# Kernel tuning notes

Hardware: AMD Instinct MI355X
Metric: run time of the kernel (lower is better)

## Reference

```python
import jax, jax.numpy as jnp
import numpy as np

B, T, U, D, V = 8, 200, 100, 512, 1024


def setup_inputs() -> dict:
    key = jax.random.key(0)
    k1, k2, k3, k4 = jax.random.split(key, 4)
    enc_out = jax.random.normal(k1, (B, T, D), dtype=jnp.float32)
    prefix = jax.random.randint(k2, (B, U), 0, V, dtype=jnp.int64)
    embedding = jax.random.normal(k3, (V, D), dtype=jnp.float32)
    joiner_w = jax.random.normal(k4, (V, D), dtype=jnp.float32) * (1.0 / np.sqrt(D))
    joiner_b = jnp.zeros((V,), dtype=jnp.float32)
    return {"enc_out": enc_out, "prefix": prefix, "embedding": embedding,
            "joiner_w": joiner_w, "joiner_b": joiner_b}


def reference(enc_out, prefix, embedding, joiner_w, joiner_b):
    # pred_emb: (B, U, D) via embedding lookup
    pred_emb = embedding[prefix]
    # broadcast add -> (B, T, U, D), then tanh
    joint = jnp.tanh(enc_out[:, :, None, :] + pred_emb[:, None, :, :])
    # linear projection to vocab: (B, T, U, V)
    logits = jnp.einsum('btud,vd->btuv', joint, joiner_w) + joiner_b
    return logits
```

## Files before the change

kernel.cpp:

```cpp
#include <hip/hip_runtime.h>

#define T_DIM 200
#define U_DIM 100
#define D_DIM 512
#define V_DIM 1024
#define TU_DIM (T_DIM * U_DIM)
#define M_TOTAL (8 * TU_DIM)
#define M_TILE 64

typedef __attribute__((ext_vector_type(8))) short bf16x8;
typedef __attribute__((ext_vector_type(4))) float f32x4;

__device__ __forceinline__ unsigned short f2bf(float f) {
    unsigned int u = __float_as_uint(f);
    u += 0x7FFFu + ((u >> 16) & 1u);
    return (unsigned short)(u >> 16);
}

__device__ __forceinline__ float fast_tanh(float x) {
    float e = __expf(2.0f * x);
    return 1.0f - 2.0f / (e + 1.0f);
}

__device__ __forceinline__ void row_ptrs(int g, const float* enc, const int* prefix,
                                         const float* emb, const float** encp, const float** embp) {
    const int b = g / TU_DIM;
    const int m = g - b * TU_DIM;
    const int t = m / U_DIM;
    const int u = m - t * U_DIM;
    *encp = enc + (size_t)(b * T_DIM + t) * D_DIM;
    *embp = emb + (size_t)prefix[b * U_DIM + u] * D_DIM;
}

__global__ void conv_w_kernel(const float* __restrict__ w, ushort4* __restrict__ wbf) {
    int i = blockIdx.x * blockDim.x + threadIdx.x;
    float4 v = reinterpret_cast<const float4*>(w)[i];
    ushort4 o;
    o.x = f2bf(v.x); o.y = f2bf(v.y); o.z = f2bf(v.z); o.w = f2bf(v.w);
    wbf[i] = o;
}

__global__ __launch_bounds__(512)
void mat_a_kernel(const float* __restrict__ enc, const int* __restrict__ prefix,
                  const float* __restrict__ emb, unsigned short* __restrict__ Abf) {
    const int tid = threadIdx.x;
    const int r = tid >> 3;
    const int q = tid & 7;
    const int rl = blockIdx.x * 64 + r;
    const float *encp, *embp;
    row_ptrs(rl, enc, prefix, emb, &encp, &embp);
    unsigned short* ap = Abf + (size_t)rl * D_DIM;
#pragma unroll
    for (int jj = 0; jj < 8; ++jj) {
        const int d = q * 8 + jj * 64;
        float4 e0 = *reinterpret_cast<const float4*>(encp + d);
        float4 e1 = *reinterpret_cast<const float4*>(encp + d + 4);
        float4 p0 = *reinterpret_cast<const float4*>(embp + d);
        float4 p1 = *reinterpret_cast<const float4*>(embp + d + 4);
        bf16x8 pk;
        pk[0] = (short)f2bf(fast_tanh(e0.x + p0.x));
        pk[1] = (short)f2bf(fast_tanh(e0.y + p0.y));
        pk[2] = (short)f2bf(fast_tanh(e0.z + p0.z));
        pk[3] = (short)f2bf(fast_tanh(e0.w + p0.w));
        pk[4] = (short)f2bf(fast_tanh(e1.x + p1.x));
        pk[5] = (short)f2bf(fast_tanh(e1.y + p1.y));
        pk[6] = (short)f2bf(fast_tanh(e1.z + p1.z));
        pk[7] = (short)f2bf(fast_tanh(e1.w + p1.w));
        *reinterpret_cast<bf16x8*>(&ap[d]) = pk;
    }
}

#define GLOAD_LDS16(gp, lp) \
    __builtin_amdgcn_global_load_lds( \
        (const __attribute__((address_space(1))) unsigned int*)(gp), \
        (__attribute__((address_space(3))) unsigned int*)(lp), 16, 0, 0)

__global__ __launch_bounds__(512, 2)
void gemm8_kernel(const unsigned short* __restrict__ Abf, const unsigned short* __restrict__ wbf,
                  const float* __restrict__ bias, float* __restrict__ out) {
    __shared__ unsigned short ldsA[2][256 * 64];
    __shared__ unsigned short ldsB[2][256 * 64];

    const int tid  = threadIdx.x;
    const int lane = tid & 63;
    const int wid  = tid >> 6;
    const int wm   = wid >> 2;
    const int wn   = wid & 3;
    const int lr   = lane & 15;
    const int lg   = lane >> 4;

    const int orig = blockIdx.x;
    const int xcd = orig & 7;
    const int wgid = (xcd < 4 ? xcd * 313 : 4 * 313 + (xcd - 4) * 312) + (orig >> 3);
    const int mt = wgid >> 2, nt = wgid & 3;
    const int row0 = mt * 256, col0 = nt * 256;

    const int rsub = tid >> 3;
    const int csw  = ((tid & 7) ^ (rsub & 7)) * 8;

    const unsigned short* aSt = Abf + (size_t)(row0 + rsub) * D_DIM + csw;
    const unsigned short* wSt = wbf + (size_t)(col0 + rsub) * D_DIM + csw;

    const unsigned short* ldsA0 = &ldsA[0][(wm * 128 + lr) * 64 + ((lg ^ (lr & 7)) * 8)];
    const unsigned short* ldsB0 = &ldsB[0][(wn * 64 + lr) * 64 + ((lg ^ (lr & 7)) * 8)];
    const int kk1off = ((((4 | lg) ^ (lr & 7)) - (lg ^ (lr & 7))) * 8);

    f32x4 acc[8][4];
#pragma unroll
    for (int mi = 0; mi < 8; ++mi)
#pragma unroll
        for (int ni = 0; ni < 4; ++ni)
            acc[mi][ni] = (f32x4){0.f, 0.f, 0.f, 0.f};

    auto stage = [&](int buf) {
#pragma unroll
        for (int j = 0; j < 4; ++j)
            GLOAD_LDS16(aSt + (size_t)j * (64 * D_DIM), &ldsA[buf][(j * 64 + wid * 8) * 64]);
#pragma unroll
        for (int j = 0; j < 4; ++j)
            GLOAD_LDS16(wSt + (size_t)j * (64 * D_DIM), &ldsB[buf][(j * 64 + wid * 8) * 64]);
        aSt += 64;
        wSt += 64;
    };

    auto compute = [&](int buf) {
        const unsigned short* pA = ldsA0 + buf * (256 * 64);
        const unsigned short* pB = ldsB0 + buf * (256 * 64);
#pragma unroll
        for (int kk = 0; kk < 2; ++kk) {
            const int ko = kk ? kk1off : 0;
            bf16x8 bfr[4];
#pragma unroll
            for (int ni = 0; ni < 4; ++ni)
                bfr[ni] = *reinterpret_cast<const bf16x8*>(pB + ni * (16 * 64) + ko);
            __builtin_amdgcn_s_setprio(1);
#pragma unroll
            for (int mi = 0; mi < 8; ++mi) {
                bf16x8 af = *reinterpret_cast<const bf16x8*>(pA + mi * (16 * 64) + ko);
#pragma unroll
                for (int ni = 0; ni < 4; ++ni)
                    acc[mi][ni] = __builtin_amdgcn_mfma_f32_16x16x32_bf16(af, bfr[ni], acc[mi][ni], 0, 0, 0);
            }
            __builtin_amdgcn_s_setprio(0);
        }
    };

    stage(0);
    stage(1);

#pragma unroll 1
    for (int it = 0; it < 4; ++it) {
        asm volatile("s_waitcnt vmcnt(8)" ::: "memory");
        __builtin_amdgcn_s_barrier();
        compute(0);
        asm volatile("s_waitcnt lgkmcnt(0)" ::: "memory");
        __builtin_amdgcn_s_barrier();
        if (it < 3) stage(0);
        if (it < 3) asm volatile("s_waitcnt vmcnt(8)" ::: "memory");
        else        asm volatile("s_waitcnt vmcnt(0)" ::: "memory");
        __builtin_amdgcn_s_barrier();
        compute(1);
        if (it < 3) {
            asm volatile("s_waitcnt lgkmcnt(0)" ::: "memory");
            __builtin_amdgcn_s_barrier();
            stage(1);
        }
    }

    float bv[4];
#pragma unroll
    for (int ni = 0; ni < 4; ++ni)
        bv[ni] = bias[col0 + wn * 64 + ni * 16 + lr];
#pragma unroll
    for (int mi = 0; mi < 8; ++mi) {
#pragma unroll
        for (int j = 0; j < 4; ++j) {
            const long long row = (long long)row0 + wm * 128 + mi * 16 + lg * 4 + j;
            float* op = out + row * V_DIM + col0 + wn * 64;
#pragma unroll
            for (int ni = 0; ni < 4; ++ni)
                __builtin_nontemporal_store(acc[mi][ni][j] + bv[ni], &op[ni * 16 + lr]);
        }
    }
}

__global__ __launch_bounds__(512, 2)
void joiner_kernel(const float* __restrict__ enc, const int* __restrict__ prefix,
                   const float* __restrict__ emb, const unsigned short* __restrict__ wbf,
                   const float* __restrict__ bias, float* __restrict__ out) {
    __shared__ unsigned short A_s[M_TILE * 512];
    const int tid = threadIdx.x;
    const long long g0 = (long long)blockIdx.x * M_TILE;
    {
        const int r = tid >> 3, q = tid & 7;
        const float *encp, *embp;
        row_ptrs((int)g0 + r, enc, prefix, emb, &encp, &embp);
        const int r7 = r & 7;
#pragma unroll
        for (int jj = 0; jj < 8; ++jj) {
            const int d = q * 8 + jj * 64;
            float4 e0 = *reinterpret_cast<const float4*>(encp + d);
            float4 e1 = *reinterpret_cast<const float4*>(encp + d + 4);
            float4 p0 = *reinterpret_cast<const float4*>(embp + d);
            float4 p1 = *reinterpret_cast<const float4*>(embp + d + 4);
            bf16x8 pk;
            pk[0] = (short)f2bf(fast_tanh(e0.x + p0.x));
            pk[1] = (short)f2bf(fast_tanh(e0.y + p0.y));
            pk[2] = (short)f2bf(fast_tanh(e0.z + p0.z));
            pk[3] = (short)f2bf(fast_tanh(e0.w + p0.w));
            pk[4] = (short)f2bf(fast_tanh(e1.x + p1.x));
            pk[5] = (short)f2bf(fast_tanh(e1.y + p1.y));
            pk[6] = (short)f2bf(fast_tanh(e1.z + p1.z));
            pk[7] = (short)f2bf(fast_tanh(e1.w + p1.w));
            const int chunk = (q + 8 * jj) ^ r7;
            *reinterpret_cast<bf16x8*>(&A_s[r * 512 + chunk * 8]) = pk;
        }
    }
    __syncthreads();
    const int lane = tid & 63, wid = tid >> 6;
    const int wn = wid * 128, lr = lane & 15, lg = lane >> 4;
    const unsigned short* wb = wbf + (size_t)(wn + lr) * D_DIM + lg * 8;
    f32x4 acc[4][8];
#pragma unroll
    for (int mi = 0; mi < 4; ++mi)
#pragma unroll
        for (int ni = 0; ni < 8; ++ni) acc[mi][ni] = (f32x4){0.f, 0.f, 0.f, 0.f};
    bf16x8 bb[2][8];
#pragma unroll
    for (int ni = 0; ni < 8; ++ni)
        bb[0][ni] = *reinterpret_cast<const bf16x8*>(wb + ni * 16 * D_DIM);
#pragma unroll
    for (int s = 0; s < 16; ++s) {
        const int cur = s & 1, nxt = cur ^ 1;
        if (s < 15) {
#pragma unroll
            for (int ni = 0; ni < 8; ++ni)
                bb[nxt][ni] = *reinterpret_cast<const bf16x8*>(wb + ni * 16 * D_DIM + (s + 1) * 32);
        }
        bf16x8 af[4];
#pragma unroll
        for (int mi = 0; mi < 4; ++mi) {
            const int row = mi * 16 + lr;
            const int chunk = (s * 4 + lg) ^ (row & 7);
            af[mi] = *reinterpret_cast<const bf16x8*>(&A_s[row * 512 + chunk * 8]);
        }
#pragma unroll
        for (int mi = 0; mi < 4; ++mi)
#pragma unroll
            for (int ni = 0; ni < 8; ++ni)
                acc[mi][ni] = __builtin_amdgcn_mfma_f32_16x16x32_bf16(af[mi], bb[cur][ni], acc[mi][ni], 0, 0, 0);
    }
    float bv[8];
#pragma unroll
    for (int ni = 0; ni < 8; ++ni) bv[ni] = bias[wn + ni * 16 + lr];
#pragma unroll
    for (int mi = 0; mi < 4; ++mi) {
#pragma unroll
        for (int j = 0; j < 4; ++j) {
            const long long row = g0 + mi * 16 + lg * 4 + j;
            float* op = out + row * V_DIM + wn;
#pragma unroll
            for (int ni = 0; ni < 8; ++ni)
                op[ni * 16 + lr] = acc[mi][ni][j] + bv[ni];
        }
    }
}

extern "C" void kernel_launch(void* const* d_in, const int* in_sizes, int n_in,
                              void* d_out, int out_size, void* d_ws, size_t ws_size,
                              hipStream_t stream) {
    const float* enc    = (const float*)d_in[0];
    const int*   prefix = (const int*)d_in[1];
    const float* emb    = (const float*)d_in[2];
    const float* jw     = (const float*)d_in[3];
    const float* jb     = (const float*)d_in[4];
    float* out = (float*)d_out;

    unsigned short* wbf = (unsigned short*)d_ws;
    const size_t WB = (size_t)V_DIM * D_DIM * sizeof(unsigned short);
    const size_t AB = (size_t)M_TOTAL * D_DIM * sizeof(unsigned short);

    conv_w_kernel<<<512, 256, 0, stream>>>(jw, (ushort4*)wbf);

    if (ws_size >= WB + AB) {
        unsigned short* Abf = wbf + (size_t)V_DIM * D_DIM;
        mat_a_kernel<<<M_TOTAL / 64, 512, 0, stream>>>(enc, prefix, emb, Abf);
        gemm8_kernel<<<2500, 512, 0, stream>>>(Abf, wbf, jb, out);
    } else {
        joiner_kernel<<<M_TOTAL / M_TILE, 512, 0, stream>>>(enc, prefix, emb, wbf, jb, out);
    }
}
```

Before: 284.0 us.

## Shrink GEMM tile to 128x128 with four waves and more workgroups

Replaces the 256x256-tile, 8-wave GEMM with a 128x128-tile, 4-wave kernel launched over 10000 workgroups, with a simpler XCD-aware remapping of block ids to tiles. Smaller tiles use less LDS and fewer registers per block. That should allow more resident blocks and better load balance across CUs, and shrink the tail of the grid. In exchange, arithmetic intensity per tile drops, so A and W are re-read from L2 more often.

```diff
diff --git a/kernel.cpp b/kernel.cpp
--- a/kernel.cpp
+++ b/kernel.cpp
@@ -75,57 +75,56 @@
         (const __attribute__((address_space(1))) unsigned int*)(gp), \
         (__attribute__((address_space(3))) unsigned int*)(lp), 16, 0, 0)
 
-__global__ __launch_bounds__(512, 2)
-void gemm8_kernel(const unsigned short* __restrict__ Abf, const unsigned short* __restrict__ wbf,
-                  const float* __restrict__ bias, float* __restrict__ out) {
-    __shared__ unsigned short ldsA[2][256 * 64];
-    __shared__ unsigned short ldsB[2][256 * 64];
+__global__ __launch_bounds__(256, 2)
+void gemm128_kernel(const unsigned short* __restrict__ Abf, const unsigned short* __restrict__ wbf,
+                    const float* __restrict__ bias, float* __restrict__ out) {
+    __shared__ unsigned short ldsA[2][128 * 64];
+    __shared__ unsigned short ldsB[2][128 * 64];
 
     const int tid  = threadIdx.x;
     const int lane = tid & 63;
     const int wid  = tid >> 6;
-    const int wm   = wid >> 2;
-    const int wn   = wid & 3;
+    const int wm   = (wid >> 1) * 64;
+    const int wn   = (wid & 1) * 64;
     const int lr   = lane & 15;
     const int lg   = lane >> 4;
 
     const int orig = blockIdx.x;
-    const int xcd = orig & 7;
-    const int wgid = (xcd < 4 ? xcd * 313 : 4 * 313 + (xcd - 4) * 312) + (orig >> 3);
-    const int mt = wgid >> 2, nt = wgid & 3;
-    const int row0 = mt * 256, col0 = nt * 256;
+    const int wgid = (orig & 7) * 1250 + (orig >> 3);
+    const int mt = wgid >> 3, nt = wgid & 7;
+    const int row0 = mt * 128, col0 = nt * 128;
 
     const int rsub = tid >> 3;
     const int csw  = ((tid & 7) ^ (rsub & 7)) * 8;
-
     const unsigned short* aSt = Abf + (size_t)(row0 + rsub) * D_DIM + csw;
     const unsigned short* wSt = wbf + (size_t)(col0 + rsub) * D_DIM + csw;
 
-    const unsigned short* ldsA0 = &ldsA[0][(wm * 128 + lr) * 64 + ((lg ^ (lr & 7)) * 8)];
-    const unsigned short* ldsB0 = &ldsB[0][(wn * 64 + lr) * 64 + ((lg ^ (lr & 7)) * 8)];
+    auto stage = [&](int buf, int kt) {
+        const int k0 = kt * 64;
+#pragma unroll
+        for (int i = 0; i < 4; ++i)
+            GLOAD_LDS16(aSt + (size_t)(i * 32) * D_DIM + k0,
+                        &ldsA[buf][(i * 32 + wid * 8) * 64]);
+#pragma unroll
+        for (int i = 0; i < 4; ++i)
+            GLOAD_LDS16(wSt + (size_t)(i * 32) * D_DIM + k0,
+                        &ldsB[buf][(i * 32 + wid * 8) * 64]);
+    };
+
+    const unsigned short* ldsA0 = &ldsA[0][(wm + lr) * 64 + ((lg ^ (lr & 7)) * 8)];
+    const unsigned short* ldsB0 = &ldsB[0][(wn + lr) * 64 + ((lg ^ (lr & 7)) * 8)];
     const int kk1off = ((((4 | lg) ^ (lr & 7)) - (lg ^ (lr & 7))) * 8);
 
-    f32x4 acc[8][4];
-#pragma unroll
-    for (int mi = 0; mi < 8; ++mi)
+    f32x4 acc[4][4];
+#pragma unroll
+    for (int mi = 0; mi < 4; ++mi)
 #pragma unroll
         for (int ni = 0; ni < 4; ++ni)
             acc[mi][ni] = (f32x4){0.f, 0.f, 0.f, 0.f};
 
-    auto stage = [&](int buf) {
-#pragma unroll
-        for (int j = 0; j < 4; ++j)
-            GLOAD_LDS16(aSt + (size_t)j * (64 * D_DIM), &ldsA[buf][(j * 64 + wid * 8) * 64]);
-#pragma unroll
-        for (int j = 0; j < 4; ++j)
-            GLOAD_LDS16(wSt + (size_t)j * (64 * D_DIM), &ldsB[buf][(j * 64 + wid * 8) * 64]);
-        aSt += 64;
-        wSt += 64;
-    };
-
     auto compute = [&](int buf) {
-        const unsigned short* pA = ldsA0 + buf * (256 * 64);
-        const unsigned short* pB = ldsB0 + buf * (256 * 64);
+        const unsigned short* pA = ldsA0 + buf * (128 * 64);
+        const unsigned short* pB = ldsB0 + buf * (128 * 64);
 #pragma unroll
         for (int kk = 0; kk < 2; ++kk) {
             const int ko = kk ? kk1off : 0;
@@ -135,7 +134,7 @@
                 bfr[ni] = *reinterpret_cast<const bf16x8*>(pB + ni * (16 * 64) + ko);
             __builtin_amdgcn_s_setprio(1);
 #pragma unroll
-            for (int mi = 0; mi < 8; ++mi) {
+            for (int mi = 0; mi < 4; ++mi) {
                 bf16x8 af = *reinterpret_cast<const bf16x8*>(pA + mi * (16 * 64) + ko);
 #pragma unroll
                 for (int ni = 0; ni < 4; ++ni)
@@ -145,8 +144,8 @@
         }
     };
 
-    stage(0);
-    stage(1);
+    stage(0, 0);
+    stage(1, 1);
 
 #pragma unroll 1
     for (int it = 0; it < 4; ++it) {
@@ -155,7 +154,7 @@
         compute(0);
         asm volatile("s_waitcnt lgkmcnt(0)" ::: "memory");
         __builtin_amdgcn_s_barrier();
-        if (it < 3) stage(0);
+        if (it < 3) stage(0, 2 * it + 2);
         if (it < 3) asm volatile("s_waitcnt vmcnt(8)" ::: "memory");
         else        asm volatile("s_waitcnt vmcnt(0)" ::: "memory");
         __builtin_amdgcn_s_barrier();
@@ -163,20 +162,20 @@
         if (it < 3) {
             asm volatile("s_waitcnt lgkmcnt(0)" ::: "memory");
             __builtin_amdgcn_s_barrier();
-            stage(1);
+            stage(1, 2 * it + 3);
         }
     }
 
     float bv[4];
 #pragma unroll
     for (int ni = 0; ni < 4; ++ni)
-        bv[ni] = bias[col0 + wn * 64 + ni * 16 + lr];
-#pragma unroll
-    for (int mi = 0; mi < 8; ++mi) {
+        bv[ni] = bias[col0 + wn + ni * 16 + lr];
+#pragma unroll
+    for (int mi = 0; mi < 4; ++mi) {
 #pragma unroll
         for (int j = 0; j < 4; ++j) {
-            const long long row = (long long)row0 + wm * 128 + mi * 16 + lg * 4 + j;
-            float* op = out + row * V_DIM + col0 + wn * 64;
+            const long long row = (long long)row0 + wm + mi * 16 + lg * 4 + j;
+            float* op = out + row * V_DIM + col0 + wn;
 #pragma unroll
             for (int ni = 0; ni < 4; ++ni)
                 __builtin_nontemporal_store(acc[mi][ni][j] + bv[ni], &op[ni * 16 + lr]);
@@ -285,7 +284,7 @@
     if (ws_size >= WB + AB) {
         unsigned short* Abf = wbf + (size_t)V_DIM * D_DIM;
         mat_a_kernel<<<M_TOTAL / 64, 512, 0, stream>>>(enc, prefix, emb, Abf);
-        gemm8_kernel<<<2500, 512, 0, stream>>>(Abf, wbf, jb, out);
+        gemm128_kernel<<<10000, 256, 0, stream>>>(Abf, wbf, jb, out);
     } else {
         joiner_kernel<<<M_TOTAL / M_TILE, 512, 0, stream>>>(enc, prefix, emb, wbf, jb, out);
     }
```

After: 276.5 us, median of 2. 1.03x faster.
